# Performance work log

Measured on AMD Instinct MI355X. Metric: run time of the kernel, lower is better.

The kernel has to match this reference:

```python
import jax, jax.numpy as jnp
import numpy as np
import math

D = 192            # base channel dim (init arg d); s has D channels
D2 = 2 * D         # y has 2d channels
H = 48; W = 48; BS = 2
NH = 8             # attention heads (divides both D2 and D)
NY = H * W         # tokens per image


def pe2d(d_model, height, width):
    """Faithful port of positionalencoding2d: (d_model, H, W)."""
    dh = d_model // 2
    div = jnp.exp(jnp.arange(0.0, dh, 2.0) * (-math.log(10000.0) / dh))  # (dh/2,)
    pw = jnp.arange(0.0, width)[:, None] * div    # (W, dh/2)
    ph = jnp.arange(0.0, height)[:, None] * div   # (H, dh/2)
    pe = jnp.zeros((d_model, height, width), jnp.float32)
    pe = pe.at[0:dh:2].set(jnp.broadcast_to(jnp.sin(pw).T[:, None, :], (dh // 2, height, width)))
    pe = pe.at[1:dh:2].set(jnp.broadcast_to(jnp.cos(pw).T[:, None, :], (dh // 2, height, width)))
    pe = pe.at[dh::2].set(jnp.broadcast_to(jnp.sin(ph).T[:, :, None], (dh // 2, height, width)))
    pe = pe.at[dh + 1::2].set(jnp.broadcast_to(jnp.cos(ph).T[:, :, None], (dh // 2, height, width)))
    return pe


def conv1x1(x, w, b):
    # x: (b,c,h,w), w: (out,c)
    return jnp.einsum('bchw,oc->bohw', x, w) + b[None, :, None, None]


def conv3x3(x, w, b):
    out = jax.lax.conv_general_dilated(x, w, (1, 1), 'SAME',
                                       dimension_numbers=('NCHW', 'OIHW', 'NCHW'))
    return out + b[None, :, None, None]


def bn(x, g, b):
    # inference-mode batchnorm with zero-mean / unit-var running stats
    return x * g[None, :, None, None] + b[None, :, None, None]


def setup_inputs() -> dict:
    key = jax.random.key(0)
    ks = jax.random.split(key, 8)
    r = lambda k, shp: jax.random.normal(k, shp, jnp.float32) * 0.02
    return {
        'y': jax.random.normal(ks[0], (BS, D2, H, W), jnp.float32),
        's': jax.random.normal(ks[1], (BS, D, H, W), jnp.float32),
        'wq_w': r(ks[2], (D2, D2)), 'wq_b': jnp.zeros((D2,), jnp.float32),
        'wk_w': r(ks[3], (D2, D2)), 'wk_b': jnp.zeros((D2,), jnp.float32),
        'wv_w': r(ks[4], (D, D)),   'wv_b': jnp.zeros((D,), jnp.float32),
        'conv1_w': r(ks[5], (D2, D2)), 'conv1_b': jnp.zeros((D2,), jnp.float32),
        'bn1_g': jnp.ones((D2,), jnp.float32), 'bn1_b': jnp.zeros((D2,), jnp.float32),
        'conv2_w': r(ks[6], (D, D)), 'conv2_b': jnp.zeros((D,), jnp.float32),
        'bn2_g': jnp.ones((D,), jnp.float32), 'bn2_b': jnp.zeros((D,), jnp.float32),
        'up_w': r(ks[7], (D2, D2, 3, 3)), 'up_b': jnp.zeros((D2,), jnp.float32),
        'conv3_w': r(jax.random.fold_in(key, 10), (D, D2)), 'conv3_b': jnp.zeros((D,), jnp.float32),
        'bn3_g': jnp.ones((D,), jnp.float32), 'bn3_b': jnp.zeros((D,), jnp.float32),
        'sig_w': r(jax.random.fold_in(key, 11), (D, D)), 'sig_b': jnp.zeros((D,), jnp.float32),
        'bnsig_g': jnp.ones((D,), jnp.float32), 'bnsig_b': jnp.zeros((D,), jnp.float32),
    }


def reference(y, s, wq_w, wq_b, wk_w, wk_b, wv_w, wv_b,
              conv1_w, conv1_b, bn1_g, bn1_b,
              conv2_w, conv2_b, bn2_g, bn2_b,
              up_w, up_b, conv3_w, conv3_b, bn3_g, bn3_b,
              sig_w, sig_b, bnsig_g, bnsig_b):
    bs = y.shape[0]
    y = y + pe2d(D2, H, W)[None]
    s = s + pe2d(D, H, W)[None]
    # conv+BN+ReLU feature extraction
    y_c1 = jax.nn.relu(bn(conv1x1(y, conv1_w, conv1_b), bn1_g, bn1_b))
    s_c2 = jax.nn.relu(bn(conv1x1(s, conv2_w, conv2_b), bn2_g, bn2_b))
    y_c3 = conv3x3(y, up_w, up_b)                                   # 'up' branch conv
    y_c3 = jax.nn.relu(bn(conv1x1(y_c3, conv3_w, conv3_b), bn3_g, bn3_b))  # (b, D, H, W)
    # tokenize
    yt = y_c1.reshape(bs, D2, NY).transpose(0, 2, 1)   # (b, ny, 2d)
    st = s_c2.reshape(bs, D, NY).transpose(0, 2, 1)    # (b, ny, d)
    # multi-head cross attention: Q,K from y-tokens, V from s-tokens
    Q = (yt @ wq_w.T + wq_b).reshape(bs, NY, NH, D2 // NH).transpose(0, 2, 1, 3)  # (b,h,ny,2d/h)
    K = (yt @ wk_w.T + wk_b).reshape(bs, NY, NH, D2 // NH).transpose(0, 2, 1, 3)
    V = (st @ wv_w.T + wv_b).reshape(bs, NY, NH, D // NH).transpose(0, 2, 1, 3)   # (b,h,ny,d/h)
    M = jnp.einsum('bhnd,bhmd->bhnm', Q, K) / math.sqrt(D)  # scale = d**0.5 as in source
    A = jax.nn.softmax(M, axis=-1)
    Z = jnp.einsum('bhnm,bhmd->bhnd', A, V)                 # (b,h,ny,d/h)
    Z = Z.transpose(0, 2, 1, 3).reshape(bs, NY, D).transpose(0, 2, 1).reshape(bs, D, H, W)
    # sigmoid gate and fuse
    g = jax.nn.sigmoid(bn(conv1x1(Z, sig_w, sig_b), bnsig_g, bnsig_b))
    Z = g * s
    return jnp.concatenate([Z, y_c3], axis=1)               # (b, 2d, H, W)
```

## Files before the change

### kernel.cpp

```cpp
#include <hip/hip_runtime.h>
#include <hip/hip_bf16.h>

#define Dc   192
#define D2c  384
#define NYc  2304

#define QSCALE 0.1041175462f

typedef __attribute__((ext_vector_type(8))) short short8;
typedef __attribute__((ext_vector_type(4))) float f32x4;

__device__ __forceinline__ unsigned short f2bf(float f) {
    unsigned int u = __float_as_uint(f);
    u += 0x7FFFu + ((u >> 16) & 1u);
    return (unsigned short)(u >> 16);
}
__device__ __forceinline__ float fexp2(float x) {
    float r; asm("v_exp_f32 %0, %1" : "=v"(r) : "v"(x)); return r;
}
__device__ __forceinline__ unsigned cvtpk(float lo, float hi) {
    unsigned r; asm("v_cvt_pk_bf16_f32 %0, %1, %2" : "=v"(r) : "v"(lo), "v"(hi));
    return r;
}

__device__ __forceinline__ float pe_val(int c, int n, int C) {
    int x = n % 48, y = n / 48;
    int dh = C >> 1;
    float pos; int i;
    if (c < dh) { i = c >> 1;        pos = (float)x; }
    else        { i = (c - dh) >> 1; pos = (float)y; }
    float divv = expf((float)(2 * i) * (-9.210340371976184f / (float)dh));
    float ang = pos * divv;
    return (c & 1) ? cosf(ang) : sinf(ang);
}

__global__ __launch_bounds__(256)
void pe_y_kernel(const float* __restrict__ y, unsigned short* __restrict__ ytok) {
    int idx = blockIdx.x * 256 + threadIdx.x;
    int n = idx % NYc; int c = (idx / NYc) % D2c; int b = idx / (NYc * D2c);
    float v = y[idx] + pe_val(c, n, D2c);
    ytok[(long)b * NYc * D2c + (long)n * D2c + c] = f2bf(v);
}

__global__ __launch_bounds__(256)
void pe_s_kernel(const float* __restrict__ s, unsigned short* __restrict__ stok,
                 float* __restrict__ sch) {
    int idx = blockIdx.x * 256 + threadIdx.x;
    int n = idx % NYc; int c = (idx / NYc) % Dc; int b = idx / (NYc * Dc);
    float v = s[idx] + pe_val(c, n, Dc);
    sch[idx] = v;
    stok[(long)b * NYc * Dc + (long)n * Dc + c] = f2bf(v);
}

__global__ __launch_bounds__(256)
void cvt_w_kernel(const float* __restrict__ w0, const float* __restrict__ w1,
                  const float* __restrict__ w2, const float* __restrict__ w3,
                  const float* __restrict__ w4, const float* __restrict__ w5,
                  const float* __restrict__ w6, unsigned short* __restrict__ dst,
                  const float* __restrict__ wq_b, const float* __restrict__ wk_b,
                  float* __restrict__ qkb) {
    int idx = blockIdx.x * 256 + threadIdx.x;
    if (idx < 768)
        qkb[idx] = (idx < 384) ? wq_b[idx] * QSCALE : wk_b[idx - 384];
    const float* src; int off; float scl = 1.0f;
    if      (idx < 147456) { src = w0; off = idx; }
    else if (idx < 294912) { src = w1; off = idx - 147456; scl = QSCALE; }
    else if (idx < 442368) { src = w2; off = idx - 294912; }
    else if (idx < 479232) { src = w3; off = idx - 442368; }
    else if (idx < 516096) { src = w4; off = idx - 479232; }
    else if (idx < 552960) { src = w5; off = idx - 516096; }
    else                   { src = w6; off = idx - 552960; }
    dst[idx] = f2bf(src[off] * scl);
}

__global__ __launch_bounds__(256)
void cvt_up_kernel(const float* __restrict__ w, unsigned short* __restrict__ wt) {
    int idx = blockIdx.x * 256 + threadIdx.x;
    int o = idx / 3456; int r = idx % 3456;
    int tap = r / 384;  int c = r % 384;
    wt[idx] = f2bf(w[((long)o * 384 + c) * 9 + tap]);
}

enum { E_BIAS = 0, E_BNRELU = 1, E_BNRELU_F32 = 2, E_SIG_F32 = 3 };

template<int EPI, bool IM2COL, bool CH_M>
__global__ __launch_bounds__(256)
void mfma_gemm(const unsigned short* __restrict__ Ar, long aBatch, int aPitch,
               const unsigned short* __restrict__ Br, long bBatch, int bPitch,
               int K,
               const float* __restrict__ bias, const float* __restrict__ bng,
               const float* __restrict__ bnb,
               const float* __restrict__ smul, long smulBatch,
               void* __restrict__ outv, long oBatch, int oPitch)
{
    int b = blockIdx.z;
    const unsigned short* A = Ar + (long)b * aBatch;
    const unsigned short* B = Br + (long)b * bBatch;
    int n0 = blockIdx.x * 64, m0 = blockIdx.y * 64;

    __shared__ __align__(16) unsigned short As[64][72];
    __shared__ __align__(16) unsigned short Bs[64][72];

    int t = threadIdx.x;
    int lane = t & 63, w = t >> 6;
    int lr = lane & 15, lg = lane >> 4;
    int wm = (w >> 1) * 32, wn = (w & 1) * 32;

    f32x4 zero = {0.f, 0.f, 0.f, 0.f};
    f32x4 acc[2][2] = {{zero, zero}, {zero, zero}};

    for (int k0 = 0; k0 < K; k0 += 64) {
        #pragma unroll
        for (int i = 0; i < 2; ++i) {
            int idx = t + i * 256;
            int row = idx >> 3, sl = idx & 7;
            uint4 av;
            if (!IM2COL) {
                av = *(const uint4*)(A + (long)(m0 + row) * aPitch + k0 + sl * 8);
            } else {
                int gk = k0 + sl * 8;
                int tap = gk / 384;
                int rem = gk - tap * 384;
                int tok = m0 + row;
                int py = tok / 48 + tap / 3 - 1;
                int px = tok % 48 + tap % 3 - 1;
                av = (py >= 0 && py < 48 && px >= 0 && px < 48)
                        ? *(const uint4*)(A + (long)(py * 48 + px) * aPitch + rem)
                        : make_uint4(0, 0, 0, 0);
            }
            uint4 bv = *(const uint4*)(B + (long)(n0 + row) * bPitch + k0 + sl * 8);
            *(uint4*)&As[row][sl * 8] = av;
            *(uint4*)&Bs[row][sl * 8] = bv;
        }
        __syncthreads();
        #pragma unroll
        for (int kk = 0; kk < 2; ++kk) {
            short8 a0 = *(const short8*)&As[wm + lr][kk * 32 + lg * 8];
            short8 a1 = *(const short8*)&As[wm + 16 + lr][kk * 32 + lg * 8];
            short8 b0 = *(const short8*)&Bs[wn + lr][kk * 32 + lg * 8];
            short8 b1 = *(const short8*)&Bs[wn + 16 + lr][kk * 32 + lg * 8];
            acc[0][0] = __builtin_amdgcn_mfma_f32_16x16x32_bf16(a0, b0, acc[0][0], 0, 0, 0);
            acc[0][1] = __builtin_amdgcn_mfma_f32_16x16x32_bf16(a0, b1, acc[0][1], 0, 0, 0);
            acc[1][0] = __builtin_amdgcn_mfma_f32_16x16x32_bf16(a1, b0, acc[1][0], 0, 0, 0);
            acc[1][1] = __builtin_amdgcn_mfma_f32_16x16x32_bf16(a1, b1, acc[1][1], 0, 0, 0);
        }
        __syncthreads();
    }

    float* outF = (float*)outv;
    unsigned short* outH = (unsigned short*)outv;
    long ob = (long)b * oBatch;
    #pragma unroll
    for (int i = 0; i < 2; ++i)
    #pragma unroll
    for (int j = 0; j < 2; ++j)
    #pragma unroll
    for (int r = 0; r < 4; ++r) {
        int gm = m0 + wm + i * 16 + lg * 4 + r;
        int gn = n0 + wn + j * 16 + lr;
        int ch = CH_M ? gm : gn;
        float v = acc[i][j][r] + bias[ch];
        if (EPI == E_BNRELU || EPI == E_BNRELU_F32)
            v = fmaxf(fmaf(v, bng[ch], bnb[ch]), 0.f);
        if (EPI == E_SIG_F32) {
            v = fmaf(v, bng[ch], bnb[ch]);
            v = 1.f / (1.f + __expf(-v));
            v *= smul[(long)b * smulBatch + (long)gm * NYc + gn];
        }
        long o = ob + (long)gm * oPitch + gn;
        if (EPI == E_BNRELU_F32 || EPI == E_SIG_F32) outF[o] = v;
        else                                         outH[o] = f2bf(v);
    }
}

__global__ __launch_bounds__(512)
void attn_kernel(const unsigned short* __restrict__ QK,
                 const unsigned short* __restrict__ Vc,
                 unsigned short* __restrict__ Zt)
{
    int qb = blockIdx.x;
    int bh = blockIdx.y;
    int b = bh >> 3, h = bh & 7;
    const unsigned short* Qg = QK + (long)b * NYc * 768 + h * 48;
    const unsigned short* Kg = Qg + 384;
    const unsigned short* Vg = Vc + ((long)b * Dc + h * 24) * NYc;
    unsigned short*       Z  = Zt + (long)b * NYc * Dc + h * 24;

    __shared__ __align__(16) unsigned short Ks_[128][72];
    __shared__ __align__(16) unsigned short Vs_[32][136];
    __shared__ __align__(16) unsigned int   Ps_[8][16][36];

    int t = threadIdx.x, lane = t & 63, w = t >> 6;
    int lr = lane & 15, lg = lane >> 4;
    int tm = w >> 1, hf = w & 1;
    int q0 = qb * 64;

    short8 z8 = {0, 0, 0, 0, 0, 0, 0, 0};
    const unsigned short* qrow = Qg + (long)(q0 + tm * 16 + lr) * 768;
    short8 bq0 = *(const short8*)(qrow + lg * 8);
    short8 bq1 = (lg < 2) ? *(const short8*)(qrow + 32 + lg * 8) : z8;

    float m_run = -1e30f, l_run = 0.f;
    f32x4 O0 = {0.f, 0.f, 0.f, 0.f}, O1 = {0.f, 0.f, 0.f, 0.f};

    for (int kt = 0; kt < 18; ++kt) {
        long k0 = kt * 128;
        #pragma unroll
        for (int i = 0; i < 2; ++i) {
            int idx = t + i * 512;
            int row = idx >> 3, sl = idx & 7;
            uint4 v = make_uint4(0, 0, 0, 0);
            if (sl < 6) v = *(const uint4*)(Kg + (k0 + row) * 768 + sl * 8);
            *(uint4*)&Ks_[row][sl * 8] = v;
        }
        if (t < 384) {
            int row = t >> 4, sl = t & 15;
            *(uint4*)&Vs_[row][sl * 8] =
                *(const uint4*)(Vg + (long)row * NYc + k0 + sl * 8);
        }
        __syncthreads();

        f32x4 sS[4];
        #pragma unroll
        for (int ks = 0; ks < 4; ++ks) {
            short8 ak0 = *(const short8*)&Ks_[hf * 64 + ks * 16 + lr][lg * 8];
            short8 ak1 = *(const short8*)&Ks_[hf * 64 + ks * 16 + lr][32 + lg * 8];
            f32x4 c = {0.f, 0.f, 0.f, 0.f};
            c = __builtin_amdgcn_mfma_f32_16x16x32_bf16(ak0, bq0, c, 0, 0, 0);
            c = __builtin_amdgcn_mfma_f32_16x16x32_bf16(ak1, bq1, c, 0, 0, 0);
            sS[ks] = c;
        }

        float tmax = -1e30f;
        #pragma unroll
        for (int ks = 0; ks < 4; ++ks)
            #pragma unroll
            for (int r = 0; r < 4; ++r) tmax = fmaxf(tmax, sS[ks][r]);
        tmax = fmaxf(tmax, __shfl_xor(tmax, 16));
        tmax = fmaxf(tmax, __shfl_xor(tmax, 32));

        if (__any(tmax > m_run + 10.f)) {
            float mn = fmaxf(m_run, tmax);
            float al = fexp2(m_run - mn);
            m_run = mn;
            l_run *= al;
            #pragma unroll
            for (int rr = 0; rr < 4; ++rr) {
                float arr = __shfl(al, (lane & 48) | (lg * 4 + rr));
                O0[rr] *= arr; O1[rr] *= arr;
            }
        }

        float psum = 0.f;
        #pragma unroll
        for (int ks = 0; ks < 4; ++ks) {
            float p0 = fexp2(sS[ks][0] - m_run);
            float p1 = fexp2(sS[ks][1] - m_run);
            float p2 = fexp2(sS[ks][2] - m_run);
            float p3 = fexp2(sS[ks][3] - m_run);
            psum += (p0 + p1) + (p2 + p3);
            Ps_[w][lr][8 * ks + 2 * lg]     = cvtpk(p0, p1);
            Ps_[w][lr][8 * ks + 2 * lg + 1] = cvtpk(p2, p3);
        }
        psum += __shfl_xor(psum, 16);
        psum += __shfl_xor(psum, 32);
        l_run += psum;

        short8 ap0 = *(const short8*)&Ps_[w][lr][4 * lg];
        short8 ap1 = *(const short8*)&Ps_[w][lr][16 + 4 * lg];
        short8 bv00 = *(const short8*)&Vs_[lr][hf * 64 + lg * 8];
        short8 bv01 = *(const short8*)&Vs_[lr][hf * 64 + 32 + lg * 8];
        short8 bv10 = *(const short8*)&Vs_[16 + lr][hf * 64 + lg * 8];
        short8 bv11 = *(const short8*)&Vs_[16 + lr][hf * 64 + 32 + lg * 8];
        O0 = __builtin_amdgcn_mfma_f32_16x16x32_bf16(ap0, bv00, O0, 0, 0, 0);
        O0 = __builtin_amdgcn_mfma_f32_16x16x32_bf16(ap1, bv01, O0, 0, 0, 0);
        O1 = __builtin_amdgcn_mfma_f32_16x16x32_bf16(ap0, bv10, O1, 0, 0, 0);
        O1 = __builtin_amdgcn_mfma_f32_16x16x32_bf16(ap1, bv11, O1, 0, 0, 0);
        __syncthreads();
    }

    float* Cf = (float*)&Ps_[0][0][0];
    float* T = Cf + tm * 576;
    if (hf == 1) {
        #pragma unroll
        for (int j = 0; j < 4; ++j) {
            T[lane * 8 + j]     = O0[j];
            T[lane * 8 + 4 + j] = O1[j];
        }
        if (lane < 16) { T[512 + lane] = m_run; T[528 + lane] = l_run; }
    }
    __syncthreads();
    if (hf == 0) {
        float mB = T[512 + lr], lB = T[528 + lr];
        float mS = fmaxf(m_run, mB);
        float aA = fexp2(m_run - mS), aB = fexp2(mB - mS);
        float invl = 1.f / (l_run * aA + lB * aB);
        float fA = aA * invl, fB = aB * invl;
        #pragma unroll
        for (int rr = 0; rr < 4; ++rr) {
            int src = (lane & 48) | (lg * 4 + rr);
            float gA = __shfl(fA, src), gB = __shfl(fB, src);
            int n = q0 + tm * 16 + lg * 4 + rr;
            unsigned short* zr = Z + (long)n * Dc;
            float z0 = O0[rr] * gA + T[lane * 8 + rr] * gB;
            zr[lr] = f2bf(z0);
            if (lr < 8) {
                float z1 = O1[rr] * gA + T[lane * 8 + 4 + rr] * gB;
                zr[16 + lr] = f2bf(z1);
            }
        }
    }
}

extern "C" void kernel_launch(void* const* d_in, const int* in_sizes, int n_in,
                              void* d_out, int out_size, void* d_ws, size_t ws_size,
                              hipStream_t stream) {
    const float* y       = (const float*)d_in[0];
    const float* s       = (const float*)d_in[1];
    const float* wq_w    = (const float*)d_in[2];
    const float* wq_b    = (const float*)d_in[3];
    const float* wk_w    = (const float*)d_in[4];
    const float* wk_b    = (const float*)d_in[5];
    const float* wv_w    = (const float*)d_in[6];
    const float* wv_b    = (const float*)d_in[7];
    const float* conv1_w = (const float*)d_in[8];
    const float* conv1_b = (const float*)d_in[9];
    const float* bn1_g   = (const float*)d_in[10];
    const float* bn1_b   = (const float*)d_in[11];
    const float* conv2_w = (const float*)d_in[12];
    const float* conv2_b = (const float*)d_in[13];
    const float* bn2_g   = (const float*)d_in[14];
    const float* bn2_b   = (const float*)d_in[15];
    const float* up_w    = (const float*)d_in[16];
    const float* up_b    = (const float*)d_in[17];
    const float* conv3_w = (const float*)d_in[18];
    const float* conv3_b = (const float*)d_in[19];
    const float* bn3_g   = (const float*)d_in[20];
    const float* bn3_b   = (const float*)d_in[21];
    const float* sig_w   = (const float*)d_in[22];
    const float* sig_b   = (const float*)d_in[23];
    const float* bnsig_g = (const float*)d_in[24];
    const float* bnsig_b = (const float*)d_in[25];

    unsigned short* wsp  = (unsigned short*)d_ws;
    unsigned short* wcvt  = wsp;
    unsigned short* upwt  = wcvt + 626688;
    unsigned short* y_pe  = upwt + 1327104;
    unsigned short* s_pe  = y_pe + 1769472;
    unsigned short* y_c1  = s_pe + 884736;
    unsigned short* s_c2  = y_c1 + 1769472;
    unsigned short* y_up  = s_c2 + 884736;
    unsigned short* QKtok = y_up + 1769472;
    unsigned short* Vch   = QKtok + 3538944;
    unsigned short* Ztok  = Vch + 884736;
    float*          s_ch  = (float*)(Ztok + 884736);
    float*          qkb   = s_ch + 884736;

    const unsigned short* conv1wb = wcvt;
    const unsigned short* wqkb    = wcvt + 147456;
    const unsigned short* conv2wb = wcvt + 442368;
    const unsigned short* wvb     = wcvt + 479232;
    const unsigned short* sigwb   = wcvt + 516096;
    const unsigned short* conv3wb = wcvt + 552960;

    const long SY2 = (long)D2c * NYc;
    const long SY1 = (long)Dc * NYc;

    pe_y_kernel<<<(2 * D2c * NYc) / 256, 256, 0, stream>>>(y, y_pe);
    pe_s_kernel<<<(2 * Dc * NYc) / 256, 256, 0, stream>>>(s, s_pe, s_ch);
    cvt_w_kernel<<<626688 / 256, 256, 0, stream>>>(conv1_w, wq_w, wk_w, conv2_w,
                                                   wv_w, sig_w, conv3_w, wcvt,
                                                   wq_b, wk_b, qkb);
    cvt_up_kernel<<<1327104 / 256, 256, 0, stream>>>(up_w, upwt);

    dim3 blk(256);
    mfma_gemm<E_BNRELU, false, false><<<dim3(6, 36, 2), blk, 0, stream>>>(
        y_pe, SY2, D2c, conv1wb, 0, D2c, D2c,
        conv1_b, bn1_g, bn1_b, nullptr, 0, y_c1, SY2, D2c);
    mfma_gemm<E_BNRELU, false, false><<<dim3(3, 36, 2), blk, 0, stream>>>(
        s_pe, SY1, Dc, conv2wb, 0, Dc, Dc,
        conv2_b, bn2_g, bn2_b, nullptr, 0, s_c2, SY1, Dc);
    mfma_gemm<E_BIAS, true, false><<<dim3(6, 36, 2), blk, 0, stream>>>(
        y_pe, SY2, D2c, upwt, 0, 9 * D2c, 9 * D2c,
        up_b, nullptr, nullptr, nullptr, 0, y_up, SY2, D2c);
    mfma_gemm<E_BNRELU_F32, false, true><<<dim3(36, 3, 2), blk, 0, stream>>>(
        conv3wb, 0, D2c, y_up, SY2, D2c, D2c,
        conv3_b, bn3_g, bn3_b, nullptr, 0,
        (float*)d_out + (long)Dc * NYc, SY2, NYc);
    mfma_gemm<E_BIAS, false, false><<<dim3(12, 36, 2), blk, 0, stream>>>(
        y_c1, SY2, D2c, wqkb, 0, D2c, D2c,
        qkb, nullptr, nullptr, nullptr, 0, QKtok, (long)NYc * 768, 768);
    mfma_gemm<E_BIAS, false, true><<<dim3(36, 3, 2), blk, 0, stream>>>(
        wvb, 0, Dc, s_c2, SY1, Dc, Dc,
        wv_b, nullptr, nullptr, nullptr, 0, Vch, SY1, NYc);
    attn_kernel<<<dim3(36, 16), dim3(512), 0, stream>>>(QKtok, Vch, Ztok);
    mfma_gemm<E_SIG_F32, false, true><<<dim3(36, 3, 2), blk, 0, stream>>>(
        sigwb, 0, Dc, Ztok, SY1, Dc, Dc,
        sig_b, bnsig_g, bnsig_b, s_ch, SY1,
        (float*)d_out, SY2, NYc);
}
```

Measured before the change: 184.7 us.

## Enlarge GEMM tiles, add register prefetch, precompute PE table, merge prep kernels

The GEMM template now takes 128x64 or 64x128 block tiles, with larger per-wave fragments. It prefetches the next K-tile into registers so global loads overlap the MFMA work. Token-major GEMMs fold the batch into the M dimension, and the im2col path computes batch from the token index. Positional encodings come from a small precomputed table instead of per-element sin/cos/exp, and the four prep kernels are merged into three launches. Larger tiles cut the number of blocks (fewer waves filling the GPU) and raise register pressure.

```diff
diff --git a/kernel.cpp b/kernel.cpp
--- a/kernel.cpp
+++ b/kernel.cpp
@@ -23,67 +23,72 @@
     return r;
 }
 
-__device__ __forceinline__ float pe_val(int c, int n, int C) {
-    int x = n % 48, y = n / 48;
+__global__ __launch_bounds__(256)
+void build_pe_kernel(float* __restrict__ peY, float* __restrict__ peS) {
+    int idx = blockIdx.x * 256 + threadIdx.x;
+    int c, p, C; float* dst; int off;
+    if (idx < 18432) { c = idx / 48; p = idx % 48; C = 384; dst = peY; off = idx; }
+    else { int k = idx - 18432; c = k / 48; p = k % 48; C = 192; dst = peS; off = k; }
     int dh = C >> 1;
-    float pos; int i;
-    if (c < dh) { i = c >> 1;        pos = (float)x; }
-    else        { i = (c - dh) >> 1; pos = (float)y; }
+    int i = ((c < dh) ? c : c - dh) >> 1;
     float divv = expf((float)(2 * i) * (-9.210340371976184f / (float)dh));
-    float ang = pos * divv;
-    return (c & 1) ? cosf(ang) : sinf(ang);
+    float ang = (float)p * divv;
+    dst[off] = (c & 1) ? cosf(ang) : sinf(ang);
 }
 
 __global__ __launch_bounds__(256)
-void pe_y_kernel(const float* __restrict__ y, unsigned short* __restrict__ ytok) {
+void prep_pe_kernel(const float* __restrict__ y, const float* __restrict__ s,
+                    const float* __restrict__ peY, const float* __restrict__ peS,
+                    unsigned short* __restrict__ ytok, unsigned short* __restrict__ stok,
+                    float* __restrict__ sch) {
     int idx = blockIdx.x * 256 + threadIdx.x;
-    int n = idx % NYc; int c = (idx / NYc) % D2c; int b = idx / (NYc * D2c);
-    float v = y[idx] + pe_val(c, n, D2c);
-    ytok[(long)b * NYc * D2c + (long)n * D2c + c] = f2bf(v);
+    if (idx < 1769472) {
+        int n = idx % NYc; int c = (idx / NYc) % D2c; int b = idx / (NYc * D2c);
+        int pos = (c < 192) ? (n % 48) : (n / 48);
+        float v = y[idx] + peY[c * 48 + pos];
+        ytok[(long)b * NYc * D2c + (long)n * D2c + c] = f2bf(v);
+    } else {
+        int k = idx - 1769472;
+        int n = k % NYc; int c = (k / NYc) % Dc; int b = k / (NYc * Dc);
+        int pos = (c < 96) ? (n % 48) : (n / 48);
+        float v = s[k] + peS[c * 48 + pos];
+        sch[k] = v;
+        stok[(long)b * NYc * Dc + (long)n * Dc + c] = f2bf(v);
+    }
 }
 
 __global__ __launch_bounds__(256)
-void pe_s_kernel(const float* __restrict__ s, unsigned short* __restrict__ stok,
-                 float* __restrict__ sch) {
+void prep_w_kernel(const float* __restrict__ w0, const float* __restrict__ w1,
+                   const float* __restrict__ w2, const float* __restrict__ w3,
+                   const float* __restrict__ w4, const float* __restrict__ w5,
+                   const float* __restrict__ w6, unsigned short* __restrict__ dst,
+                   const float* __restrict__ wq_b, const float* __restrict__ wk_b,
+                   float* __restrict__ qkb,
+                   const float* __restrict__ upw, unsigned short* __restrict__ upwt) {
     int idx = blockIdx.x * 256 + threadIdx.x;
-    int n = idx % NYc; int c = (idx / NYc) % Dc; int b = idx / (NYc * Dc);
-    float v = s[idx] + pe_val(c, n, Dc);
-    sch[idx] = v;
-    stok[(long)b * NYc * Dc + (long)n * Dc + c] = f2bf(v);
-}
-
-__global__ __launch_bounds__(256)
-void cvt_w_kernel(const float* __restrict__ w0, const float* __restrict__ w1,
-                  const float* __restrict__ w2, const float* __restrict__ w3,
-                  const float* __restrict__ w4, const float* __restrict__ w5,
-                  const float* __restrict__ w6, unsigned short* __restrict__ dst,
-                  const float* __restrict__ wq_b, const float* __restrict__ wk_b,
-                  float* __restrict__ qkb) {
-    int idx = blockIdx.x * 256 + threadIdx.x;
-    if (idx < 768)
-        qkb[idx] = (idx < 384) ? wq_b[idx] * QSCALE : wk_b[idx - 384];
-    const float* src; int off; float scl = 1.0f;
-    if      (idx < 147456) { src = w0; off = idx; }
-    else if (idx < 294912) { src = w1; off = idx - 147456; scl = QSCALE; }
-    else if (idx < 442368) { src = w2; off = idx - 294912; }
-    else if (idx < 479232) { src = w3; off = idx - 442368; }
-    else if (idx < 516096) { src = w4; off = idx - 479232; }
-    else if (idx < 552960) { src = w5; off = idx - 516096; }
-    else                   { src = w6; off = idx - 552960; }
-    dst[idx] = f2bf(src[off] * scl);
-}
-
-__global__ __launch_bounds__(256)
-void cvt_up_kernel(const float* __restrict__ w, unsigned short* __restrict__ wt) {
-    int idx = blockIdx.x * 256 + threadIdx.x;
-    int o = idx / 3456; int r = idx % 3456;
-    int tap = r / 384;  int c = r % 384;
-    wt[idx] = f2bf(w[((long)o * 384 + c) * 9 + tap]);
+    if (idx < 626688) {
+        if (idx < 768)
+            qkb[idx] = (idx < 384) ? wq_b[idx] * QSCALE : wk_b[idx - 384];
+        const float* src; int off; float scl = 1.0f;
+        if      (idx < 147456) { src = w0; off = idx; }
+        else if (idx < 294912) { src = w1; off = idx - 147456; scl = QSCALE; }
+        else if (idx < 442368) { src = w2; off = idx - 294912; }
+        else if (idx < 479232) { src = w3; off = idx - 442368; }
+        else if (idx < 516096) { src = w4; off = idx - 479232; }
+        else if (idx < 552960) { src = w5; off = idx - 516096; }
+        else                   { src = w6; off = idx - 552960; }
+        dst[idx] = f2bf(src[off] * scl);
+    } else {
+        int k = idx - 626688;
+        int o = k / 3456; int r = k % 3456;
+        int tap = r / 384;  int c = r % 384;
+        upwt[k] = f2bf(upw[((long)o * 384 + c) * 9 + tap]);
+    }
 }
 
 enum { E_BIAS = 0, E_BNRELU = 1, E_BNRELU_F32 = 2, E_SIG_F32 = 3 };
 
-template<int EPI, bool IM2COL, bool CH_M>
+template<int EPI, bool IM2COL, bool CH_M, int BMt, int BNt>
 __global__ __launch_bounds__(256)
 void mfma_gemm(const unsigned short* __restrict__ Ar, long aBatch, int aPitch,
                const unsigned short* __restrict__ Br, long bBatch, int bPitch,
@@ -93,67 +98,103 @@
                const float* __restrict__ smul, long smulBatch,
                void* __restrict__ outv, long oBatch, int oPitch)
 {
+    constexpr int MF = BMt / 32;
+    constexpr int NF = BNt / 32;
+    constexpr int LA = BMt / 32;
+    constexpr int LB = BNt / 32;
+
     int b = blockIdx.z;
     const unsigned short* A = Ar + (long)b * aBatch;
     const unsigned short* B = Br + (long)b * bBatch;
-    int n0 = blockIdx.x * 64, m0 = blockIdx.y * 64;
-
-    __shared__ __align__(16) unsigned short As[64][72];
-    __shared__ __align__(16) unsigned short Bs[64][72];
-
-    int t = threadIdx.x;
-    int lane = t & 63, w = t >> 6;
+    int m0 = blockIdx.x * BMt, n0 = blockIdx.y * BNt;
+
+    __shared__ __align__(16) unsigned short As[BMt][72];
+    __shared__ __align__(16) unsigned short Bs[BNt][72];
+
+    int t = threadIdx.x, lane = t & 63, w = t >> 6;
     int lr = lane & 15, lg = lane >> 4;
-    int wm = (w >> 1) * 32, wn = (w & 1) * 32;
-
-    f32x4 zero = {0.f, 0.f, 0.f, 0.f};
-    f32x4 acc[2][2] = {{zero, zero}, {zero, zero}};
-
-    for (int k0 = 0; k0 < K; k0 += 64) {
-        #pragma unroll
-        for (int i = 0; i < 2; ++i) {
+    int wm = (BMt == 128) ? (w >> 1) * 64 : (w & 1) * 32;
+    int wn = (BNt == 128) ? (w >> 1) * 64 : (w & 1) * 32;
+
+    f32x4 acc[MF][NF];
+    #pragma unroll
+    for (int i = 0; i < MF; ++i)
+        #pragma unroll
+        for (int j = 0; j < NF; ++j)
+            acc[i][j] = (f32x4){0.f, 0.f, 0.f, 0.f};
+
+    uint4 ra[LA], rb[LB];
+
+    auto load = [&](int k0) {
+        #pragma unroll
+        for (int i = 0; i < LA; ++i) {
+            int idx = t + i * 256, row = idx >> 3, sl = idx & 7;
+            if (!IM2COL) {
+                ra[i] = *(const uint4*)(A + (long)(m0 + row) * aPitch + k0 + sl * 8);
+            } else {
+                int tok = m0 + row;
+                int bb = (tok >= NYc) ? 1 : 0;
+                int n = tok - bb * NYc;
+                int tap = k0 / 384;
+                int rem = k0 - tap * 384 + sl * 8;
+                int py = n / 48 + tap / 3 - 1;
+                int px = n % 48 + tap % 3 - 1;
+                ra[i] = (py >= 0 && py < 48 && px >= 0 && px < 48)
+                    ? *(const uint4*)(A + ((long)bb * NYc + py * 48 + px) * aPitch + rem)
+                    : make_uint4(0, 0, 0, 0);
+            }
+        }
+        #pragma unroll
+        for (int i = 0; i < LB; ++i) {
+            int idx = t + i * 256, row = idx >> 3, sl = idx & 7;
+            rb[i] = *(const uint4*)(B + (long)(n0 + row) * bPitch + k0 + sl * 8);
+        }
+    };
+    auto store = [&]() {
+        #pragma unroll
+        for (int i = 0; i < LA; ++i) {
             int idx = t + i * 256;
-            int row = idx >> 3, sl = idx & 7;
-            uint4 av;
-            if (!IM2COL) {
-                av = *(const uint4*)(A + (long)(m0 + row) * aPitch + k0 + sl * 8);
-            } else {
-                int gk = k0 + sl * 8;
-                int tap = gk / 384;
-                int rem = gk - tap * 384;
-                int tok = m0 + row;
-                int py = tok / 48 + tap / 3 - 1;
-                int px = tok % 48 + tap % 3 - 1;
-                av = (py >= 0 && py < 48 && px >= 0 && px < 48)
-                        ? *(const uint4*)(A + (long)(py * 48 + px) * aPitch + rem)
-                        : make_uint4(0, 0, 0, 0);
-            }
-            uint4 bv = *(const uint4*)(B + (long)(n0 + row) * bPitch + k0 + sl * 8);
-            *(uint4*)&As[row][sl * 8] = av;
-            *(uint4*)&Bs[row][sl * 8] = bv;
+            *(uint4*)&As[idx >> 3][(idx & 7) * 8] = ra[i];
+        }
+        #pragma unroll
+        for (int i = 0; i < LB; ++i) {
+            int idx = t + i * 256;
+            *(uint4*)&Bs[idx >> 3][(idx & 7) * 8] = rb[i];
+        }
+    };
+
+    load(0); store(); __syncthreads();
+
+    int NT = K / 64;
+    for (int tt = 0; tt < NT; ++tt) {
+        if (tt + 1 < NT) load((tt + 1) * 64);
+        #pragma unroll
+        for (int kk = 0; kk < 2; ++kk) {
+            short8 af[MF], bf[NF];
+            #pragma unroll
+            for (int i = 0; i < MF; ++i)
+                af[i] = *(const short8*)&As[wm + i * 16 + lr][kk * 32 + lg * 8];
+            #pragma unroll
+            for (int j = 0; j < NF; ++j)
+                bf[j] = *(const short8*)&Bs[wn + j * 16 + lr][kk * 32 + lg * 8];
+            #pragma unroll
+            for (int i = 0; i < MF; ++i)
+                #pragma unroll
+                for (int j = 0; j < NF; ++j)
+                    acc[i][j] = __builtin_amdgcn_mfma_f32_16x16x32_bf16(
+                                    af[i], bf[j], acc[i][j], 0, 0, 0);
         }
         __syncthreads();
-        #pragma unroll
-        for (int kk = 0; kk < 2; ++kk) {
-            short8 a0 = *(const short8*)&As[wm + lr][kk * 32 + lg * 8];
-            short8 a1 = *(const short8*)&As[wm + 16 + lr][kk * 32 + lg * 8];
-            short8 b0 = *(const short8*)&Bs[wn + lr][kk * 32 + lg * 8];
-            short8 b1 = *(const short8*)&Bs[wn + 16 + lr][kk * 32 + lg * 8];
-            acc[0][0] = __builtin_amdgcn_mfma_f32_16x16x32_bf16(a0, b0, acc[0][0], 0, 0, 0);
-            acc[0][1] = __builtin_amdgcn_mfma_f32_16x16x32_bf16(a0, b1, acc[0][1], 0, 0, 0);
-            acc[1][0] = __builtin_amdgcn_mfma_f32_16x16x32_bf16(a1, b0, acc[1][0], 0, 0, 0);
-            acc[1][1] = __builtin_amdgcn_mfma_f32_16x16x32_bf16(a1, b1, acc[1][1], 0, 0, 0);
-        }
-        __syncthreads();
+        if (tt + 1 < NT) { store(); __syncthreads(); }
     }
 
     float* outF = (float*)outv;
     unsigned short* outH = (unsigned short*)outv;
     long ob = (long)b * oBatch;
     #pragma unroll
-    for (int i = 0; i < 2; ++i)
+    for (int i = 0; i < MF; ++i)
     #pragma unroll
-    for (int j = 0; j < 2; ++j)
+    for (int j = 0; j < NF; ++j)
     #pragma unroll
     for (int r = 0; r < 4; ++r) {
         int gm = m0 + wm + i * 16 + lg * 4 + r;
@@ -342,7 +383,7 @@
     const float* bnsig_g = (const float*)d_in[24];
     const float* bnsig_b = (const float*)d_in[25];
 
-    unsigned short* wsp  = (unsigned short*)d_ws;
+    unsigned short* wsp   = (unsigned short*)d_ws;
     unsigned short* wcvt  = wsp;
     unsigned short* upwt  = wcvt + 626688;
     unsigned short* y_pe  = upwt + 1327104;
@@ -355,6 +396,8 @@
     unsigned short* Ztok  = Vch + 884736;
     float*          s_ch  = (float*)(Ztok + 884736);
     float*          qkb   = s_ch + 884736;
+    float*          peY   = qkb + 768;
+    float*          peS   = peY + 18432;
 
     const unsigned short* conv1wb = wcvt;
     const unsigned short* wqkb    = wcvt + 147456;
@@ -366,35 +409,34 @@
     const long SY2 = (long)D2c * NYc;
     const long SY1 = (long)Dc * NYc;
 
-    pe_y_kernel<<<(2 * D2c * NYc) / 256, 256, 0, stream>>>(y, y_pe);
-    pe_s_kernel<<<(2 * Dc * NYc) / 256, 256, 0, stream>>>(s, s_pe, s_ch);
-    cvt_w_kernel<<<626688 / 256, 256, 0, stream>>>(conv1_w, wq_w, wk_w, conv2_w,
-                                                   wv_w, sig_w, conv3_w, wcvt,
-                                                   wq_b, wk_b, qkb);
-    cvt_up_kernel<<<1327104 / 256, 256, 0, stream>>>(up_w, upwt);
+    build_pe_kernel<<<108, 256, 0, stream>>>(peY, peS);
+    prep_pe_kernel<<<10368, 256, 0, stream>>>(y, s, peY, peS, y_pe, s_pe, s_ch);
+    prep_w_kernel<<<7632, 256, 0, stream>>>(conv1_w, wq_w, wk_w, conv2_w,
+                                            wv_w, sig_w, conv3_w, wcvt,
+                                            wq_b, wk_b, qkb, up_w, upwt);
 
     dim3 blk(256);
-    mfma_gemm<E_BNRELU, false, false><<<dim3(6, 36, 2), blk, 0, stream>>>(
-        y_pe, SY2, D2c, conv1wb, 0, D2c, D2c,
-        conv1_b, bn1_g, bn1_b, nullptr, 0, y_c1, SY2, D2c);
-    mfma_gemm<E_BNRELU, false, false><<<dim3(3, 36, 2), blk, 0, stream>>>(
-        s_pe, SY1, Dc, conv2wb, 0, Dc, Dc,
-        conv2_b, bn2_g, bn2_b, nullptr, 0, s_c2, SY1, Dc);
-    mfma_gemm<E_BIAS, true, false><<<dim3(6, 36, 2), blk, 0, stream>>>(
-        y_pe, SY2, D2c, upwt, 0, 9 * D2c, 9 * D2c,
-        up_b, nullptr, nullptr, nullptr, 0, y_up, SY2, D2c);
-    mfma_gemm<E_BNRELU_F32, false, true><<<dim3(36, 3, 2), blk, 0, stream>>>(
+    mfma_gemm<E_BNRELU, false, false, 128, 64><<<dim3(36, 6, 1), blk, 0, stream>>>(
+        y_pe, 0, D2c, conv1wb, 0, D2c, D2c,
+        conv1_b, bn1_g, bn1_b, nullptr, 0, y_c1, 0, D2c);
+    mfma_gemm<E_BNRELU, false, false, 128, 64><<<dim3(36, 3, 1), blk, 0, stream>>>(
+        s_pe, 0, Dc, conv2wb, 0, Dc, Dc,
+        conv2_b, bn2_g, bn2_b, nullptr, 0, s_c2, 0, Dc);
+    mfma_gemm<E_BIAS, true, false, 128, 64><<<dim3(36, 6, 1), blk, 0, stream>>>(
+        y_pe, 0, D2c, upwt, 0, 9 * D2c, 9 * D2c,
+        up_b, nullptr, nullptr, nullptr, 0, y_up, 0, D2c);
+    mfma_gemm<E_BNRELU_F32, false, true, 64, 128><<<dim3(3, 18, 2), blk, 0, stream>>>(
         conv3wb, 0, D2c, y_up, SY2, D2c, D2c,
         conv3_b, bn3_g, bn3_b, nullptr, 0,
         (float*)d_out + (long)Dc * NYc, SY2, NYc);
-    mfma_gemm<E_BIAS, false, false><<<dim3(12, 36, 2), blk, 0, stream>>>(
-        y_c1, SY2, D2c, wqkb, 0, D2c, D2c,
-        qkb, nullptr, nullptr, nullptr, 0, QKtok, (long)NYc * 768, 768);
-    mfma_gemm<E_BIAS, false, true><<<dim3(36, 3, 2), blk, 0, stream>>>(
+    mfma_gemm<E_BIAS, false, false, 128, 64><<<dim3(36, 12, 1), blk, 0, stream>>>(
+        y_c1, 0, D2c, wqkb, 0, D2c, D2c,
+        qkb, nullptr, nullptr, nullptr, 0, QKtok, 0, 768);
+    mfma_gemm<E_BIAS, false, true, 64, 128><<<dim3(3, 18, 2), blk, 0, stream>>>(
         wvb, 0, Dc, s_c2, SY1, Dc, Dc,
         wv_b, nullptr, nullptr, nullptr, 0, Vch, SY1, NYc);
     attn_kernel<<<dim3(36, 16), dim3(512), 0, stream>>>(QKtok, Vch, Ztok);
-    mfma_gemm<E_SIG_F32, false, true><<<dim3(36, 3, 2), blk, 0, stream>>>(
+    mfma_gemm<E_SIG_F32, false, true, 64, 128><<<dim3(3, 18, 2), blk, 0, stream>>>(
         sigwb, 0, Dc, Ztok, SY1, Dc, Dc,
         sig_b, bnsig_g, bnsig_b, s_ch, SY1,
         (float*)d_out, SY2, NYc);
```

New measurement: 226.8 us. 22.8% more time.
